# Optimization experiments

Measured on AMD Instinct MI355X. Metric: run time of the kernel, lower is better.

Reference implementation:

```python
import jax, jax.numpy as jnp
from jax import lax
import numpy as np

ROI = 7  # roi_size


def _extract_rois(feat, coords):
    """Faithful port of extract_roi_features: clamp a 7x7 window to image bounds,
    then bilinearly resize the (possibly smaller) crop back to 7x7
    (F.interpolate, mode='bilinear', align_corners=False)."""
    B, C, H, W = feat.shape
    half = ROI // 2

    def axis_idx(c, size):
        start = jnp.maximum(0, c - half)                  # [B,A]
        end = jnp.minimum(size, c + half + 1)
        Li = end - start                                  # crop length (int) [B,A]
        L = Li.astype(feat.dtype)[..., None]              # [B,A,1]
        j = jnp.arange(ROI, dtype=feat.dtype)
        # align_corners=False source coordinate, clamped into the crop
        src = jnp.clip((j + 0.5) * L / ROI - 0.5, 0.0, L - 1.0)  # [B,A,7]
        i0 = jnp.floor(src).astype(jnp.int32)
        i1 = jnp.minimum(i0 + 1, Li[..., None] - 1)
        w1 = src - i0.astype(feat.dtype)
        return start[..., None] + i0, start[..., None] + i1, 1.0 - w1, w1

    xc = coords[..., 0].astype(jnp.int32)
    yc = coords[..., 1].astype(jnp.int32)
    y0, y1, wy0, wy1 = axis_idx(yc, H)
    x0, x1, wx0, wx1 = axis_idx(xc, W)
    Bn, A = xc.shape
    bi = jnp.arange(Bn)[:, None, None, None]

    def g(Y, X):  # gather -> [B,A,7,7,C]
        return feat[bi, :, Y[:, :, :, None], X[:, :, None, :]]

    wy0 = wy0[:, :, :, None, None]; wy1 = wy1[:, :, :, None, None]
    wx0 = wx0[:, :, None, :, None]; wx1 = wx1[:, :, None, :, None]
    v = (wy0 * wx0 * g(y0, x0) + wy0 * wx1 * g(y0, x1)
         + wy1 * wx0 * g(y1, x0) + wy1 * wx1 * g(y1, x1))
    return jnp.transpose(v, (0, 1, 4, 2, 3))  # [B,A,C,7,7]


def _conv(x, w, b, pad):
    y = lax.conv_general_dilated(x, w, (1, 1), [(pad, pad), (pad, pad)],
                                 dimension_numbers=('NCHW', 'OIHW', 'NCHW'))
    return y + b[None, :, None, None]


def _bn(x, scale, bias, mean, var, eps=1e-5):
    inv = scale * lax.rsqrt(var + eps)
    return x * inv[None, :, None, None] + (bias - mean * inv)[None, :, None, None]


def setup_inputs() -> dict:
    key = jax.random.key(0)
    ks = jax.random.split(key, 12)
    B, A, C, H, W = 8, 128, 256, 64, 64
    f32 = jnp.float32
    d = {}
    d['feat_rgb'] = jax.random.normal(ks[0], (B, C, H, W), f32)
    d['feat_tir'] = jax.random.normal(ks[1], (B, C, H, W), f32)
    d['anchor_coords'] = jax.random.randint(ks[2], (B, A, 2), 0, 64).astype(jnp.int32)
    # local_fusion: Conv(2C->C,3) BN ReLU Conv(C->C,3) BN ReLU
    d['conv1_w'] = jax.random.normal(ks[3], (C, 2 * C, 3, 3), f32) * 0.02
    d['conv1_b'] = jnp.zeros((C,), f32)
    d['bn1_scale'] = jnp.ones((C,), f32)
    d['bn1_bias'] = jnp.zeros((C,), f32)
    d['bn1_mean'] = jax.random.normal(ks[4], (C,), f32) * 0.1
    d['bn1_var'] = jax.random.uniform(ks[5], (C,), f32, 0.5, 1.5)
    d['conv2_w'] = jax.random.normal(ks[6], (C, C, 3, 3), f32) * 0.02
    d['conv2_b'] = jnp.zeros((C,), f32)
    d['bn2_scale'] = jnp.ones((C,), f32)
    d['bn2_bias'] = jnp.zeros((C,), f32)
    d['bn2_mean'] = jax.random.normal(ks[7], (C,), f32) * 0.1
    d['bn2_var'] = jax.random.uniform(ks[8], (C,), f32, 0.5, 1.5)
    # weight_generator: Conv(C->C//4,1) ReLU Conv(C//4->2,1) Softmax(dim=1)
    d['wg1_w'] = jax.random.normal(ks[9], (C // 4, C, 1, 1), f32) * 0.05
    d['wg1_b'] = jnp.zeros((C // 4,), f32)
    d['wg2_w'] = jax.random.normal(ks[10], (2, C // 4, 1, 1), f32) * 0.05
    d['wg2_b'] = jnp.zeros((2,), f32)
    return d


def reference(feat_rgb, feat_tir, anchor_coords,
              conv1_w, conv1_b, bn1_scale, bn1_bias, bn1_mean, bn1_var,
              conv2_w, conv2_b, bn2_scale, bn2_bias, bn2_mean, bn2_var,
              wg1_w, wg1_b, wg2_w, wg2_b):
    B, C, H, W = feat_rgb.shape
    A = anchor_coords.shape[1]
    roi_rgb = _extract_rois(feat_rgb, anchor_coords)  # [B,A,C,7,7]
    roi_tir = _extract_rois(feat_tir, anchor_coords)
    rgb = roi_rgb.reshape(B * A, C, ROI, ROI)
    tir = roi_tir.reshape(B * A, C, ROI, ROI)
    x = jnp.concatenate([rgb, tir], axis=1)           # [B*A, 2C, 7, 7]
    x = jax.nn.relu(_bn(_conv(x, conv1_w, conv1_b, 1), bn1_scale, bn1_bias, bn1_mean, bn1_var))
    x = jax.nn.relu(_bn(_conv(x, conv2_w, conv2_b, 1), bn2_scale, bn2_bias, bn2_mean, bn2_var))
    h = jax.nn.relu(_conv(x, wg1_w, wg1_b, 0))
    w = jax.nn.softmax(_conv(h, wg2_w, wg2_b, 0), axis=1)  # [B*A, 2, 7, 7]
    fused = w[:, 0:1] * rgb + w[:, 1:2] * tir
    return fused.reshape(B, A, C, ROI, ROI)
```

## Files before the change

kernel.cpp:

```cpp
#include <hip/hip_runtime.h>
#include <cstddef>
#include <cstdint>


typedef unsigned int u32;
typedef unsigned short u16;
typedef __attribute__((ext_vector_type(8))) short short8;
typedef __attribute__((ext_vector_type(4))) float float4v;

__device__ __forceinline__ float bf2f(u16 u) {
  u32 x = ((u32)u) << 16;
  return __builtin_bit_cast(float, x);
}
__device__ __forceinline__ u16 f2bf(float f) {
  u32 x = __builtin_bit_cast(u32, f);
  x = x + 0x7fffu + ((x >> 16) & 1u);
  return (u16)(x >> 16);
}
__device__ __forceinline__ void gl_lds16(const void* g, void* l) {
  __builtin_amdgcn_global_load_lds((const __attribute__((address_space(1))) void*)g,
                                   (__attribute__((address_space(3))) void*)l, 16, 0, 0);
}

template <int IC>
__global__ void k_prep_w(const float* __restrict__ w, u16* __restrict__ wt) {
  int i = blockIdx.x * 256 + threadIdx.x;
  if (i >= 9 * 256 * IC) return;
  int t = i / (256 * IC);
  int rem = i - t * 256 * IC;
  int oc = rem / IC, ic = rem - oc * IC;
  wt[i] = f2bf(w[((size_t)oc * IC + ic) * 9 + t]);
}

__global__ void k_prep_bn(const float* __restrict__ cb, const float* __restrict__ sc,
                          const float* __restrict__ bi, const float* __restrict__ mn,
                          const float* __restrict__ vr, float* __restrict__ sb) {
  int c = threadIdx.x;
  float inv = sc[c] * rsqrtf(vr[c] + 1e-5f);
  sb[c]       = inv;
  sb[256 + c] = cb[c] * inv + (bi[c] - mn[c] * inv);
}

__global__ __launch_bounds__(256)
void k_roi2(const float* __restrict__ frgb, const float* __restrict__ ftir,
            const int* __restrict__ coords, u16* __restrict__ cat) {
  int ba = blockIdx.x, b = ba >> 7, tid = threadIdx.x;
  __shared__ int   si0[2][7], si1[2][7];
  __shared__ float sw0[2][7], sw1[2][7];
  __shared__ u16 tile[49][514];
  if (tid < 14) {
    int axis = tid / 7;
    int j = tid - axis * 7;
    int c = coords[ba * 2 + (axis == 0 ? 1 : 0)];
    int start = max(0, c - 3);
    int end   = min(64, c + 4);
    int Li = end - start;
    float L = (float)Li;
    float src = ((float)j + 0.5f) * L / 7.0f - 0.5f;
    src = fminf(fmaxf(src, 0.0f), L - 1.0f);
    int i0 = (int)floorf(src);
    int i1 = min(i0 + 1, Li - 1);
    float w1 = src - (float)i0;
    si0[axis][j] = start + i0;
    si1[axis][j] = start + i1;
    sw0[axis][j] = 1.0f - w1;
    sw1[axis][j] = w1;
  }
  __syncthreads();
  const float* fr = frgb + (size_t)b * 256 * 4096;
  const float* ft = ftir + (size_t)b * 256 * 4096;
  for (int idx = tid; idx < 256 * 49; idx += 256) {
    int c = idx / 49, p = idx - c * 49;
    int jy = p / 7, jx = p - (p / 7) * 7;
    int y0 = si0[0][jy], y1 = si1[0][jy];
    int x0 = si0[1][jx], x1 = si1[1][jx];
    float wy0 = sw0[0][jy], wy1 = sw1[0][jy];
    float wx0 = sw0[1][jx], wx1 = sw1[1][jx];
    float a00 = wy0 * wx0, a01 = wy0 * wx1, a10 = wy1 * wx0, a11 = wy1 * wx1;
    const float* fc = fr + (size_t)c * 4096;
    float vr_ = a00 * fc[y0 * 64 + x0] + a01 * fc[y0 * 64 + x1] +
                a10 * fc[y1 * 64 + x0] + a11 * fc[y1 * 64 + x1];
    const float* gc = ft + (size_t)c * 4096;
    float vt_ = a00 * gc[y0 * 64 + x0] + a01 * gc[y0 * 64 + x1] +
                a10 * gc[y1 * 64 + x0] + a11 * gc[y1 * 64 + x1];
    tile[p][c]       = f2bf(vr_);
    tile[p][256 + c] = f2bf(vt_);
  }
  __syncthreads();
  u16* dst = cat + (size_t)ba * 81 * 512;
  for (int o = tid; o < 81 * 512; o += 256) {
    int row = o >> 9, c = o & 511;
    int py0 = row / 9, px0 = row - (row / 9) * 9;
    u16 v = 0;
    if (py0 >= 1 && py0 <= 7 && px0 >= 1 && px0 <= 7)
      v = tile[(py0 - 1) * 7 + (px0 - 1)][c];
    dst[o] = v;
  }
}

template <int ICT, bool FIRST>
__global__ __launch_bounds__(512, 4)
void k_conv_mfma(const u16* __restrict__ IN, const u16* __restrict__ WT,
                 const float* __restrict__ sb, u16* __restrict__ OUT) {
  constexpr int NC = ICT / 64;
  constexpr int BUFB = 2 * 81 * 128;
  __shared__ __align__(16) u16 lds[2][BUFB / 2];
  const int tid = threadIdx.x;
  const int lane = tid & 63, wv = tid >> 6;
  const int l15 = lane & 15, hi = lane >> 4;
  const int ba2 = blockIdx.x * 2;
  const char* inb = (const char*)IN;

  if (FIRST) {
    int oc = tid & 255, rh = tid >> 8;
    u16* ob = OUT + ((size_t)(ba2 + rh) * 81) * 256 + oc;
#pragma unroll
    for (int i = 0; i < 32; ++i) {
      int row = (i < 9) ? i : (i < 18) ? (63 + i)
                                       : (9 * ((i - 18) / 2 + 1) + ((i - 18) & 1) * 8);
      ob[row * 256] = 0;
    }
  }

  int rg[7];
#pragma unroll
  for (int pf = 0; pf < 7; ++pf) {
    int P = pf * 16 + l15;
    if (P > 97) P = 97;
    int roi = (P >= 49) ? 1 : 0;
    int q = P - roi * 49;
    rg[pf] = roi * 81 + (q / 7) * 9 + (q - (q / 7) * 7);
  }

  float4v acc[7][2];
#pragma unroll
  for (int a = 0; a < 7; ++a)
#pragma unroll
    for (int f = 0; f < 2; ++f) acc[a][f] = (float4v){0.f, 0.f, 0.f, 0.f};

  auto stage = [&](int ch, int buf) {
    for (int s = wv; s < 21; s += 8) {
      int d = s * 1024 + lane * 16;
      if (d < BUFB) {
        int u = d ^ (((d >> 7) & 7) << 4);
        int row_g = u >> 7;
        int col = u & 127;
        int roi = (row_g >= 81) ? 1 : 0;
        int rr = row_g - roi * 81;
        const char* src = inb + ((size_t)(ba2 + roi) * 81 + rr) * (ICT * 2) +
                          ch * 128 + col;
        gl_lds16(src, (char*)&lds[buf][0] + s * 1024);
      }
    }
  };

  stage(0, 0);
  __syncthreads();

  const int wlane = (wv * 32 + l15) * ICT + hi * 8;

  int cur = 0;
#pragma unroll 1
  for (int ch = 0; ch < NC; ++ch) {
    if (ch + 1 < NC) stage(ch + 1, cur ^ 1);
    const char* lb = (const char*)&lds[cur][0];
    const u16* wch = WT + wlane + ch * 64;
    short8 wfr[2][2];
#pragma unroll
    for (int f = 0; f < 2; ++f)
      wfr[0][f] = *(const short8*)(wch + (f * 16) * ICT);
#pragma unroll
    for (int j = 0; j < 18; ++j) {
      const int t = j >> 1, kk = j & 1;
      const int dy = t / 3, dx = t - (t / 3) * 3;
      if (j < 17) {
        const int t2 = (j + 1) >> 1, k2 = (j + 1) & 1;
#pragma unroll
        for (int f = 0; f < 2; ++f)
          wfr[(j + 1) & 1][f] =
              *(const short8*)(wch + (t2 * 256 + f * 16) * ICT + k2 * 32);
      }
      short8 bfr[7];
#pragma unroll
      for (int pf = 0; pf < 7; ++pf) {
        int rr = rg[pf] + dy * 9 + dx;
        int byt = (rr * 128 + kk * 64 + hi * 16) ^ ((rr & 7) << 4);
        bfr[pf] = *(const short8*)(lb + byt);
      }
      __builtin_amdgcn_s_setprio(1);
#pragma unroll
      for (int pf = 0; pf < 7; ++pf)
#pragma unroll
        for (int f = 0; f < 2; ++f)
          acc[pf][f] = FIRST
              ? __builtin_amdgcn_mfma_f32_16x16x32_bf16(bfr[pf], wfr[j & 1][f],
                                                        acc[pf][f], 0, 0, 0)
              : __builtin_amdgcn_mfma_f32_16x16x32_bf16(wfr[j & 1][f], bfr[pf],
                                                        acc[pf][f], 0, 0, 0);
      __builtin_amdgcn_s_setprio(0);
    }
    __syncthreads();
    cur ^= 1;
  }

  if (FIRST) {
    u16* ob = OUT + (size_t)ba2 * 81 * 256;
#pragma unroll
    for (int f = 0; f < 2; ++f) {
      int oc = wv * 32 + f * 16 + l15;
      float s = sb[oc], bb = sb[256 + oc];
#pragma unroll
      for (int pf = 0; pf < 7; ++pf)
#pragma unroll
        for (int reg = 0; reg < 4; ++reg) {
          int P = pf * 16 + hi * 4 + reg;
          if (P < 98) {
            int roi = (P >= 49) ? 1 : 0;
            int q = P - roi * 49;
            int pp = (q / 7 + 1) * 9 + (q - (q / 7) * 7) + 1;
            ob[((size_t)roi * 81 + pp) * 256 + oc] =
                f2bf(fmaxf(acc[pf][f][reg] * s + bb, 0.0f));
          }
        }
    }
  } else {
    u16* ob = OUT + (size_t)ba2 * 256 * 49;
#pragma unroll
    for (int f = 0; f < 2; ++f)
#pragma unroll
      for (int reg = 0; reg < 4; ++reg) {
        int oc = wv * 32 + f * 16 + hi * 4 + reg;
        float s = sb[oc], bb = sb[256 + oc];
#pragma unroll
        for (int pf = 0; pf < 7; ++pf) {
          int P = pf * 16 + l15;
          if (P < 98) {
            int roi = (P >= 49) ? 1 : 0;
            int q = P - roi * 49;
            ob[((size_t)roi * 256 + oc) * 49 + q] =
                f2bf(fmaxf(acc[pf][f][reg] * s + bb, 0.0f));
          }
        }
      }
  }
}

__global__ __launch_bounds__(256)
void k_head_fuse(const u16* __restrict__ x3, const u16* __restrict__ cat,
                 const float* __restrict__ w1, const float* __restrict__ b1,
                 const float* __restrict__ w2, const float* __restrict__ b2,
                 float* __restrict__ out) {
  int ba  = blockIdx.x;
  int tid = threadIdx.x;
  __shared__ float xs[256 * 49];
  __shared__ float hs[64 * 49];
  __shared__ float ls[2 * 49];
  __shared__ float swx[2 * 49];
  const u16* src = x3 + (size_t)ba * 256 * 49;
  for (int idx = tid; idx < 256 * 49; idx += 256) xs[idx] = bf2f(src[idx]);
  __syncthreads();
  for (int idx = tid; idx < 64 * 49; idx += 256) {
    int oh = idx / 49, p = idx - oh * 49;
    float s = b1[oh];
    const float* wr = w1 + oh * 256;
    for (int ic = 0; ic < 256; ++ic) s += wr[ic] * xs[ic * 49 + p];
    hs[idx] = fmaxf(s, 0.0f);
  }
  __syncthreads();
  if (tid < 98) {
    int chn = tid / 49, p = tid - chn * 49;
    float s = b2[chn];
    const float* wr = w2 + chn * 64;
    for (int k = 0; k < 64; ++k) s += wr[k] * hs[k * 49 + p];
    ls[tid] = s;
  }
  __syncthreads();
  if (tid < 49) {
    float l0 = ls[tid], l1 = ls[49 + tid];
    float m = fmaxf(l0, l1);
    float e0 = expf(l0 - m), e1 = expf(l1 - m);
    float d = e0 + e1;
    swx[tid]      = e0 / d;
    swx[49 + tid] = e1 / d;
  }
  __syncthreads();
  const u16* cr = cat + (size_t)ba * 81 * 512;
  float* o = out + (size_t)ba * 256 * 49;
  for (int idx = tid; idx < 256 * 49; idx += 256) {
    int c = idx / 49, p = idx - (idx / 49) * 49;
    int pp = (p / 7 + 1) * 9 + (p - (p / 7) * 7) + 1;
    float rgb = bf2f(cr[pp * 512 + c]);
    float tir = bf2f(cr[pp * 512 + 256 + c]);
    o[idx] = swx[p] * rgb + swx[49 + p] * tir;
  }
}

extern "C" void kernel_launch(void* const* d_in, const int* in_sizes, int n_in,
                              void* d_out, int out_size, void* d_ws, size_t ws_size,
                              hipStream_t stream) {
  const float* feat_rgb = (const float*)d_in[0];
  const float* feat_tir = (const float*)d_in[1];
  const int*   coords   = (const int*)d_in[2];
  const float* conv1_w  = (const float*)d_in[3];
  const float* conv1_b  = (const float*)d_in[4];
  const float* bn1_s    = (const float*)d_in[5];
  const float* bn1_b    = (const float*)d_in[6];
  const float* bn1_m    = (const float*)d_in[7];
  const float* bn1_v    = (const float*)d_in[8];
  const float* conv2_w  = (const float*)d_in[9];
  const float* conv2_b  = (const float*)d_in[10];
  const float* bn2_s    = (const float*)d_in[11];
  const float* bn2_b    = (const float*)d_in[12];
  const float* bn2_m    = (const float*)d_in[13];
  const float* bn2_v    = (const float*)d_in[14];
  const float* wg1_w    = (const float*)d_in[15];
  const float* wg1_b    = (const float*)d_in[16];
  const float* wg2_w    = (const float*)d_in[17];
  const float* wg2_b    = (const float*)d_in[18];
  float* out = (float*)d_out;

  char* base = (char*)d_ws;
  u16*   W1T  = (u16*)(base);
  u16*   W2T  = (u16*)(base + 2359296);
  float* SB1  = (float*)(base + 2359296 + 1179648);
  float* SB2  = (float*)(base + 2359296 + 1179648 + 2048);
  u16*   CAT2 = (u16*)(base + 2359296 + 1179648 + 4096);
  u16*   X2   = (u16*)(base + 2359296 + 1179648 + 4096 + 84934656);
  u16*   X3   = (u16*)(base + 2359296 + 1179648 + 4096 + 84934656 + 42467328);

  k_prep_w<512><<<(9 * 256 * 512 + 255) / 256, 256, 0, stream>>>(conv1_w, W1T);
  k_prep_w<256><<<(9 * 256 * 256 + 255) / 256, 256, 0, stream>>>(conv2_w, W2T);
  k_prep_bn<<<1, 256, 0, stream>>>(conv1_b, bn1_s, bn1_b, bn1_m, bn1_v, SB1);
  k_prep_bn<<<1, 256, 0, stream>>>(conv2_b, bn2_s, bn2_b, bn2_m, bn2_v, SB2);
  k_roi2<<<1024, 256, 0, stream>>>(feat_rgb, feat_tir, coords, CAT2);
  k_conv_mfma<512, true><<<512, 512, 0, stream>>>(CAT2, W1T, SB1, X2);
  k_conv_mfma<256, false><<<512, 512, 0, stream>>>(X2, W2T, SB2, X3);
  k_head_fuse<<<1024, 256, 0, stream>>>(X3, CAT2, wg1_w, wg1_b, wg2_w, wg2_b, out);
}
```

Before: 746.6 us.

## Switch conv MFMA to 32x32x16 tiles with repacked weight layout

```diff
diff --git a/kernel.cpp b/kernel.cpp
--- a/kernel.cpp
+++ b/kernel.cpp
@@ -6,7 +6,7 @@
 typedef unsigned int u32;
 typedef unsigned short u16;
 typedef __attribute__((ext_vector_type(8))) short short8;
-typedef __attribute__((ext_vector_type(4))) float float4v;
+typedef __attribute__((ext_vector_type(16))) float float16v;
 
 __device__ __forceinline__ float bf2f(u16 u) {
   u32 x = ((u32)u) << 16;
@@ -26,9 +26,13 @@
 __global__ void k_prep_w(const float* __restrict__ w, u16* __restrict__ wt) {
   int i = blockIdx.x * 256 + threadIdx.x;
   if (i >= 9 * 256 * IC) return;
-  int t = i / (256 * IC);
-  int rem = i - t * 256 * IC;
-  int oc = rem / IC, ic = rem - oc * IC;
+  int e = i & 7;
+  int r = i >> 3;
+  int oc = r & 255;
+  int r2 = r >> 8;
+  int oct = r2 % (IC / 8);
+  int t = r2 / (IC / 8);
+  int ic = oct * 8 + e;
   wt[i] = f2bf(w[((size_t)oc * IC + ic) * 9 + t]);
 }
 
@@ -107,7 +111,8 @@
   __shared__ __align__(16) u16 lds[2][BUFB / 2];
   const int tid = threadIdx.x;
   const int lane = tid & 63, wv = tid >> 6;
-  const int l15 = lane & 15, hi = lane >> 4;
+  const int ng = wv & 3, mg = wv >> 2;
+  const int l31 = lane & 31, h32 = lane >> 5;
   const int ba2 = blockIdx.x * 2;
   const char* inb = (const char*)IN;
 
@@ -122,21 +127,23 @@
     }
   }
 
-  int rg[7];
-#pragma unroll
-  for (int pf = 0; pf < 7; ++pf) {
-    int P = pf * 16 + l15;
+  int rg[2];
+#pragma unroll
+  for (int i = 0; i < 2; ++i) {
+    int P = (mg * 2 + i) * 32 + l31;
     if (P > 97) P = 97;
     int roi = (P >= 49) ? 1 : 0;
     int q = P - roi * 49;
-    rg[pf] = roi * 81 + (q / 7) * 9 + (q - (q / 7) * 7);
-  }
-
-  float4v acc[7][2];
-#pragma unroll
-  for (int a = 0; a < 7; ++a)
-#pragma unroll
-    for (int f = 0; f < 2; ++f) acc[a][f] = (float4v){0.f, 0.f, 0.f, 0.f};
+    rg[i] = roi * 81 + (q / 7) * 9 + (q - (q / 7) * 7);
+  }
+
+  float16v acc[2][2];
+#pragma unroll
+  for (int i = 0; i < 2; ++i)
+#pragma unroll
+    for (int f = 0; f < 2; ++f)
+#pragma unroll
+      for (int e = 0; e < 16; ++e) acc[i][f][e] = 0.0f;
 
   auto stage = [&](int ch, int buf) {
     for (int s = wv; s < 21; s += 8) {
@@ -157,47 +164,45 @@
   stage(0, 0);
   __syncthreads();
 
-  const int wlane = (wv * 32 + l15) * ICT + hi * 8;
+  const u16* wthr = WT + (size_t)h32 * 2048 + (size_t)(ng * 64 + l31) * 8;
 
   int cur = 0;
 #pragma unroll 1
   for (int ch = 0; ch < NC; ++ch) {
     if (ch + 1 < NC) stage(ch + 1, cur ^ 1);
     const char* lb = (const char*)&lds[cur][0];
-    const u16* wch = WT + wlane + ch * 64;
-    short8 wfr[2][2];
-#pragma unroll
-    for (int f = 0; f < 2; ++f)
-      wfr[0][f] = *(const short8*)(wch + (f * 16) * ICT);
-#pragma unroll
-    for (int j = 0; j < 18; ++j) {
-      const int t = j >> 1, kk = j & 1;
+    const u16* wch = wthr + (size_t)ch * 8 * 2048;
+#pragma unroll
+    for (int t = 0; t < 9; ++t) {
       const int dy = t / 3, dx = t - (t / 3) * 3;
-      if (j < 17) {
-        const int t2 = (j + 1) >> 1, k2 = (j + 1) & 1;
+      short8 wfr[4][2];
+#pragma unroll
+      for (int kk = 0; kk < 4; ++kk)
 #pragma unroll
         for (int f = 0; f < 2; ++f)
-          wfr[(j + 1) & 1][f] =
-              *(const short8*)(wch + (t2 * 256 + f * 16) * ICT + k2 * 32);
+          wfr[kk][f] = *(const short8*)(wch + (size_t)(t * (ICT / 8) + kk * 2) * 2048 +
+                                        f * 256);
+#pragma unroll
+      for (int kk = 0; kk < 4; ++kk) {
+        short8 bfr[2];
+#pragma unroll
+        for (int i = 0; i < 2; ++i) {
+          int rr = rg[i] + dy * 9 + dx;
+          int byt = (rr * 128 + kk * 32 + h32 * 16) ^ ((rr & 7) << 4);
+          bfr[i] = *(const short8*)(lb + byt);
+        }
+        __builtin_amdgcn_s_setprio(1);
+#pragma unroll
+        for (int i = 0; i < 2; ++i)
+#pragma unroll
+          for (int f = 0; f < 2; ++f)
+            acc[i][f] = FIRST
+                ? __builtin_amdgcn_mfma_f32_32x32x16_bf16(bfr[i], wfr[kk][f],
+                                                          acc[i][f], 0, 0, 0)
+                : __builtin_amdgcn_mfma_f32_32x32x16_bf16(wfr[kk][f], bfr[i],
+                                                          acc[i][f], 0, 0, 0);
+        __builtin_amdgcn_s_setprio(0);
       }
-      short8 bfr[7];
-#pragma unroll
-      for (int pf = 0; pf < 7; ++pf) {
-        int rr = rg[pf] + dy * 9 + dx;
-        int byt = (rr * 128 + kk * 64 + hi * 16) ^ ((rr & 7) << 4);
-        bfr[pf] = *(const short8*)(lb + byt);
-      }
-      __builtin_amdgcn_s_setprio(1);
-#pragma unroll
-      for (int pf = 0; pf < 7; ++pf)
-#pragma unroll
-        for (int f = 0; f < 2; ++f)
-          acc[pf][f] = FIRST
-              ? __builtin_amdgcn_mfma_f32_16x16x32_bf16(bfr[pf], wfr[j & 1][f],
-                                                        acc[pf][f], 0, 0, 0)
-              : __builtin_amdgcn_mfma_f32_16x16x32_bf16(wfr[j & 1][f], bfr[pf],
-                                                        acc[pf][f], 0, 0, 0);
-      __builtin_amdgcn_s_setprio(0);
     }
     __syncthreads();
     cur ^= 1;
@@ -207,41 +212,45 @@
     u16* ob = OUT + (size_t)ba2 * 81 * 256;
 #pragma unroll
     for (int f = 0; f < 2; ++f) {
-      int oc = wv * 32 + f * 16 + l15;
+      int oc = ng * 64 + f * 32 + l31;
       float s = sb[oc], bb = sb[256 + oc];
 #pragma unroll
-      for (int pf = 0; pf < 7; ++pf)
-#pragma unroll
-        for (int reg = 0; reg < 4; ++reg) {
-          int P = pf * 16 + hi * 4 + reg;
+      for (int i = 0; i < 2; ++i) {
+        int tl = mg * 2 + i;
+#pragma unroll
+        for (int reg = 0; reg < 16; ++reg) {
+          int m = (reg & 3) + 8 * (reg >> 2) + 4 * h32;
+          int P = tl * 32 + m;
           if (P < 98) {
             int roi = (P >= 49) ? 1 : 0;
             int q = P - roi * 49;
             int pp = (q / 7 + 1) * 9 + (q - (q / 7) * 7) + 1;
             ob[((size_t)roi * 81 + pp) * 256 + oc] =
-                f2bf(fmaxf(acc[pf][f][reg] * s + bb, 0.0f));
-          }
-        }
-    }
-  } else {
-    u16* ob = OUT + (size_t)ba2 * 256 * 49;
-#pragma unroll
-    for (int f = 0; f < 2; ++f)
-#pragma unroll
-      for (int reg = 0; reg < 4; ++reg) {
-        int oc = wv * 32 + f * 16 + hi * 4 + reg;
-        float s = sb[oc], bb = sb[256 + oc];
-#pragma unroll
-        for (int pf = 0; pf < 7; ++pf) {
-          int P = pf * 16 + l15;
-          if (P < 98) {
-            int roi = (P >= 49) ? 1 : 0;
-            int q = P - roi * 49;
-            ob[((size_t)roi * 256 + oc) * 49 + q] =
-                f2bf(fmaxf(acc[pf][f][reg] * s + bb, 0.0f));
+                f2bf(fmaxf(acc[i][f][reg] * s + bb, 0.0f));
           }
         }
       }
+    }
+  } else {
+    u16* ob = OUT + (size_t)ba2 * 256 * 49;
+#pragma unroll
+    for (int i = 0; i < 2; ++i) {
+      int tl = mg * 2 + i;
+      int P = tl * 32 + l31;
+      if (P < 98) {
+        int roi = (P >= 49) ? 1 : 0;
+        int q = P - roi * 49;
+#pragma unroll
+        for (int f = 0; f < 2; ++f)
+#pragma unroll
+          for (int reg = 0; reg < 16; ++reg) {
+            int oc = ng * 64 + f * 32 + (reg & 3) + 8 * (reg >> 2) + 4 * h32;
+            float s = sb[oc], bb = sb[256 + oc];
+            ob[((size_t)roi * 256 + oc) * 49 + q] =
+                f2bf(fmaxf(acc[i][f][reg] * s + bb, 0.0f));
+          }
+      }
+    }
   }
 }
 
```

Measured after the change: 616.9 us. -17.4%, faster.
